# Optimization experiments

Hardware: AMD Instinct MI355X
Metric: run time of the kernel (lower is better)

## Reference

```python
import jax, jax.numpy as jnp
import numpy as np

LMAX = 2
L = LMAX + 1          # number of l channels
M = (LMAX + 1) ** 2   # 9 spherical components
C = 64                # channels per l
N = 1024              # nodes
E = 300               # num_elements (hard-coded in module)
P3, P2, P1 = 16, 4, 2 # CG path counts for correlation 3/2/1


def so3_linear(x, w, b=None):
    # x: [N, M, Cin]; w: [L, Cout, Cin]. Per-l channel mixing (equivariant),
    # bias only on the l=0 (scalar) block.
    outs = []
    for l in range(L):
        seg = x[:, l * l:(l + 1) * (l + 1), :]
        y = jnp.einsum('nmc,dc->nmd', seg, w[l])
        if l == 0 and b is not None:
            y = y + b
        outs.append(y)
    return jnp.concatenate(outs, axis=1)


def setup_inputs() -> dict:
    key = jax.random.key(0)
    ks = jax.random.split(key, 13)
    s = lambda k, shape, sc=1.0: jax.random.normal(k, shape, dtype=jnp.float32) * sc
    return {
        'irreps_x': s(ks[0], (N, M, C)),
        'atomic_numbers': jax.random.randint(ks[1], (N,), 0, 119),
        'w_fc1': s(ks[2], (L, C, C), 1.0 / np.sqrt(C)),
        'b_fc1': jnp.zeros((C,), jnp.float32),
        'U3': s(ks[3], (M, M, M, M, P3), 0.05),   # generalized CG coeffs, corr 3
        'W3': s(ks[4], (E, P3, C), 1.0 / np.sqrt(P3 * C)),
        'U2': s(ks[5], (M, M, M, P2), 0.05),      # corr 2
        'W2': s(ks[6], (E, P2, C), 1.0 / np.sqrt(P2 * C)),
        'U1': s(ks[7], (M, M, P1), 0.05),         # corr 1
        'W1': s(ks[8], (E, P1, C), 1.0 / np.sqrt(P1 * C)),
        'w_lin': s(ks[9], (L, C, C), 1.0 / np.sqrt(C)),   # e3nn Linear in dtp block
        'w_fc2': s(ks[10], (L, C, C), 1.0 / np.sqrt(C)),  # final SO3_Linear
        'b_fc2': jnp.zeros((C,), jnp.float32),
    }


def reference(irreps_x, atomic_numbers, w_fc1, b_fc1, U3, W3, U2, W2, U1, W1,
              w_lin, w_fc2, b_fc2):
    # 1) irreps_small_fc
    x = so3_linear(irreps_x, w_fc1, b_fc1)           # [N, M, C]
    # 2) permute(0, 2, 1): MACE layout [N, C, M]
    xT = jnp.transpose(x, (0, 2, 1))
    # one_hot(atomic_numbers) @ W  ==  gather of per-element weights
    a = atomic_numbers.astype(jnp.int32)
    w3 = W3[a]                                        # [N, P3, C]
    w2 = W2[a]                                        # [N, P2, C]
    w1 = W1[a]                                        # [N, P1, C]
    # MACE symmetric contraction, correlation = 3:
    # out[n,c,o,a,b] = sum_{i,p} U3[o,a,b,i,p] * w3[n,p,c] * x[n,c,i]
    z = jnp.einsum('nci,npc->ncip', xT, w3)           # [N, C, M, P3]
    out = jnp.einsum('oabip,ncip->ncoab', U3, z)      # [N, C, M, M, M]
    # fold in correlation-2 term, contract one input index
    c2 = jnp.einsum('oaip,npc->ncoai', U2, w2)        # [N, C, M, M, M]
    out = jnp.einsum('ncoai,nci->ncoa', c2 + out, xT) # [N, C, M, M]
    # fold in correlation-1 term, contract last input index
    c1 = jnp.einsum('oip,npc->ncoi', U1, w1)          # [N, C, M, M]
    out = jnp.einsum('ncoi,nci->nco', c1 + out, xT)   # [N, C, M]
    # e3nn per-irrep Linear inside EquivariantProductBasisBlock (no bias)
    out = jnp.transpose(out, (0, 2, 1))               # back2orderTmul -> [N, M, C]
    out = so3_linear(out, w_lin)
    # 3) final SO3_Linear back to input channel count
    out = so3_linear(out, w_fc2, b_fc2)
    return out                                        # [N, M, C]
```

## Files before the change

kernel.cpp:

```cpp
#include <hip/hip_runtime.h>


typedef __attribute__((ext_vector_type(8)))  _Float16 f16x8;
typedef __attribute__((ext_vector_type(16))) float    f32x16;
typedef __attribute__((ext_vector_type(4)))  float    f32x4;
typedef __attribute__((ext_vector_type(8)))  short    short8;

static __device__ __forceinline__ unsigned short f2bf(float f) {
    union { float f; unsigned u; } v; v.f = f;
    unsigned r = v.u + 0x7fffu + ((v.u >> 16) & 1u);
    return (unsigned short)(r >> 16);
}

__global__ void prep_u3w(const float* __restrict__ U3, const float* __restrict__ U2,
                         _Float16* __restrict__ U3w)
{
    int idx = blockIdx.x * 256 + threadIdx.x;
    int ks = idx / 192, r = idx % 192;
    int nt = r >> 6, l = r & 63;
    int oa = nt * 32 + (l & 31), half = l >> 5;
    f16x8 v;
    if (ks < 81) {
        int b = ks / 9, ksub = ks % 9, ip0 = ksub * 16 + half * 8;
        #pragma unroll
        for (int j = 0; j < 8; ++j) {
            float f = (oa < 81) ? U3[(oa * 9 + b) * 144 + ip0 + j] : 0.f;
            v[j] = (_Float16)f;
        }
    } else {
        int ip0 = (ks - 81) * 16 + half * 8;
        #pragma unroll
        for (int j = 0; j < 8; ++j) {
            int ip2 = ip0 + j;
            float f = (oa < 81 && ip2 < 36) ? U2[oa * 36 + ip2] : 0.f;
            v[j] = (_Float16)f;
        }
    }
    ((f16x8*)U3w)[idx] = v;
}

__global__ __launch_bounds__(768, 3) void mace_main(
    const float* __restrict__ irreps_x,
    const int*   __restrict__ atomic_numbers,
    const float* __restrict__ w_fc1,
    const float* __restrict__ b_fc1,
    const float* __restrict__ W3,
    const float* __restrict__ W2,
    const float* __restrict__ U1,
    const float* __restrict__ W1,
    const float* __restrict__ w_lin,
    const float* __restrict__ w_fc2,
    const float* __restrict__ b_fc2,
    const _Float16* __restrict__ U3w,
    float* __restrict__ out)
{
    __shared__ float xvL[2304];
    __shared__ __align__(16) unsigned char o2B[104448];
    float* const o2L = (float*)o2B;
    float* const o1L          = (float*)o2B;
    unsigned short* const XfA = (unsigned short*)(o2B + 9216);
    unsigned short* const WfA = (unsigned short*)(o2B + 28416);
    float* const yL           = (float*)(o2B + 54016);

    const int t  = threadIdx.x;
    const int n0 = blockIdx.x * 4;
    const int w  = t >> 6;
    const int l  = t & 63;
    const int kg = l >> 4;
    const int half = l >> 5;

    auto fill_Xf = [&](auto srcf) {
        for (int i = t; i < 48 * 192; i += 768) {
            int rr = i / 192, k = i % 192;
            int lh = k >> 6, c = k & 63;
            float v = 0.f;
            if (rr < 36) {
                int at = rr / 9, m = rr % 9;
                int lm = (m >= 4) ? 2 : (m >= 1 ? 1 : 0);
                if (lh == lm) v = srcf(at, m, c);
            }
            XfA[rr * 200 + k] = f2bf(v);
        }
    };
    auto fill_Wf = [&](const float* wmat) {
        for (int i = t; i < 64 * 192; i += 768) {
            int d = i / 192, k = i % 192;
            int lh = k >> 6, c = k & 63;
            WfA[d * 200 + k] = f2bf(wmat[lh * 4096 + d * 64 + c]);
        }
    };
    auto run_linear = [&](const float* bias, float* dst, bool to_global) {
        {
            int rt = w >> 2, ct = w & 3;
            int row = rt * 16 + (l & 15);
            int col = ct * 16 + (l & 15);
            short8 A[6];
            const unsigned short* ab = XfA + row * 200 + kg * 8;
            #pragma unroll
            for (int kt = 0; kt < 6; ++kt) A[kt] = *(const short8*)(ab + kt * 32);
            const unsigned short* bb = WfA + col * 200 + kg * 8;
            f32x4 acc0 = {0,0,0,0}, acc1 = {0,0,0,0};
            #pragma unroll
            for (int kt = 0; kt < 6; kt += 2) {
                short8 B0 = *(const short8*)(bb + kt * 32);
                short8 B1 = *(const short8*)(bb + (kt + 1) * 32);
                acc0 = __builtin_amdgcn_mfma_f32_16x16x32_bf16(A[kt],     B0, acc0, 0, 0, 0);
                acc1 = __builtin_amdgcn_mfma_f32_16x16x32_bf16(A[kt + 1], B1, acc1, 0, 0, 0);
            }
            f32x4 acc = acc0 + acc1;
            #pragma unroll
            for (int r = 0; r < 4; ++r) {
                int rr = rt * 16 + kg * 4 + r;
                if (rr < 36) {
                    int at = rr / 9, m = rr % 9;
                    float v = acc[r];
                    if (bias && m == 0) v += bias[col];
                    if (to_global) dst[(n0 + at) * 576 + m * 64 + col] = v;
                    else           dst[at * 576 + m * 64 + col] = v;
                }
            }
        }
    };

    fill_Xf([&](int at, int m, int c) { return irreps_x[(n0 + at) * 576 + m * 64 + c]; });
    fill_Wf(w_fc1);
    __syncthreads();
    run_linear(b_fc1, xvL, false);
    __syncthreads();

    {
        const int at = w / 3, ng = w % 3;
        const int an = atomic_numbers[n0 + at];
        const float* xa  = xvL + at * 576;
        const float* W3r = W3 + an * 1024;
        const float* W2r = W2 + an * 256;

        f16x8 s3f[2][9], s2f[2][3];
        #pragma unroll
        for (int mt = 0; mt < 2; ++mt) {
            const int c = mt * 32 + (l & 31);
            f16x8 w3h;
            #pragma unroll
            for (int j = 0; j < 8; ++j)
                w3h[j] = (_Float16)W3r[(half * 8 + j) * 64 + c];
            #pragma unroll
            for (int i = 0; i < 9; ++i) {
                _Float16 xi = (_Float16)xa[i * 64 + c];
                f16x8 xi8 = {xi, xi, xi, xi, xi, xi, xi, xi};
                s3f[mt][i] = w3h * xi8;
            }
            float w2v[4];
            #pragma unroll
            for (int p = 0; p < 4; ++p) w2v[p] = W2r[p * 64 + c];
            #pragma unroll
            for (int ks2 = 0; ks2 < 3; ++ks2) {
                f16x8 v;
                #pragma unroll
                for (int j = 0; j < 8; ++j) {
                    int ip2 = ks2 * 16 + half * 8 + j;
                    int i = ip2 >> 2;
                    float f = (i < 9) ? xa[i * 64 + c] * w2v[ip2 & 3] : 0.f;
                    v[j] = (_Float16)f;
                }
                s2f[mt][ks2] = v;
            }
        }

        f32x16 acc0 = {0.f}, acc1 = {0.f};
        const f16x8* Bp = (const f16x8*)U3w + ng * 64 + l;
        for (int b = 0; b < 9; ++b) {
            _Float16 h0 = (_Float16)xa[b * 64 + (l & 31)];
            _Float16 h1 = (_Float16)xa[b * 64 + 32 + (l & 31)];
            f16x8 xb0 = {h0, h0, h0, h0, h0, h0, h0, h0};
            f16x8 xb1 = {h1, h1, h1, h1, h1, h1, h1, h1};
            const f16x8* Bb = Bp + b * 9 * 192;
            #pragma unroll
            for (int ksub = 0; ksub < 9; ++ksub) {
                f16x8 B = Bb[ksub * 192];
                acc0 = __builtin_amdgcn_mfma_f32_32x32x16_f16(s3f[0][ksub] * xb0, B, acc0, 0, 0, 0);
                acc1 = __builtin_amdgcn_mfma_f32_32x32x16_f16(s3f[1][ksub] * xb1, B, acc1, 0, 0, 0);
            }
        }
        #pragma unroll
        for (int ks2 = 0; ks2 < 3; ++ks2) {
            f16x8 B = Bp[(81 + ks2) * 192];
            acc0 = __builtin_amdgcn_mfma_f32_32x32x16_f16(s2f[0][ks2], B, acc0, 0, 0, 0);
            acc1 = __builtin_amdgcn_mfma_f32_32x32x16_f16(s2f[1][ks2], B, acc1, 0, 0, 0);
        }

        const int oa = ng * 32 + (l & 31);
        float* o2row = o2L + (at * 96 + oa) * 68;
        #pragma unroll
        for (int q = 0; q < 4; ++q) {
            int c0 = q * 8 + half * 4;
            f32x4 v0 = {acc0[q*4+0], acc0[q*4+1], acc0[q*4+2], acc0[q*4+3]};
            f32x4 v1 = {acc1[q*4+0], acc1[q*4+1], acc1[q*4+2], acc1[q*4+3]};
            *(f32x4*)(o2row + c0)      = v0;
            *(f32x4*)(o2row + 32 + c0) = v1;
        }
    }
    __syncthreads();

    float o1v[3];
    #pragma unroll
    for (int it = 0; it < 3; ++it) {
        int i = t + it * 768;
        int at2 = i / 576, r2 = i % 576, o = r2 >> 6, c = r2 & 63;
        int an2 = atomic_numbers[n0 + at2];
        float w1a = W1[an2 * 128 + c], w1b = W1[an2 * 128 + 64 + c];
        const float* o2p = o2L + (at2 * 96 + o * 9) * 68 + c;
        float acc = 0.f, sa = 0.f, sb = 0.f;
        #pragma unroll
        for (int a = 0; a < 9; ++a)
            acc += o2p[a * 68] * xvL[at2 * 576 + a * 64 + c];
        #pragma unroll
        for (int i2 = 0; i2 < 9; ++i2) {
            float xc = xvL[at2 * 576 + i2 * 64 + c];
            sa += U1[o * 18 + i2 * 2]     * xc;
            sb += U1[o * 18 + i2 * 2 + 1] * xc;
        }
        o1v[it] = acc + sa * w1a + sb * w1b;
    }
    __syncthreads();
    #pragma unroll
    for (int it = 0; it < 3; ++it) {
        int i = t + it * 768;
        int at2 = i / 576, r2 = i % 576;
        o1L[at2 * 576 + r2] = o1v[it];
    }
    __syncthreads();

    fill_Xf([&](int at, int m, int c) { return o1L[at * 576 + m * 64 + c]; });
    fill_Wf(w_lin);
    __syncthreads();
    run_linear(nullptr, yL, false);
    __syncthreads();

    fill_Xf([&](int at, int m, int c) { return yL[at * 576 + m * 64 + c]; });
    fill_Wf(w_fc2);
    __syncthreads();
    run_linear(b_fc2, out, true);
}

extern "C" void kernel_launch(void* const* d_in, const int* in_sizes, int n_in,
                              void* d_out, int out_size, void* d_ws, size_t ws_size,
                              hipStream_t stream) {
    const float* irreps_x = (const float*)d_in[0];
    const int*   anum     = (const int*)d_in[1];
    const float* w_fc1    = (const float*)d_in[2];
    const float* b_fc1    = (const float*)d_in[3];
    const float* U3       = (const float*)d_in[4];
    const float* W3       = (const float*)d_in[5];
    const float* U2       = (const float*)d_in[6];
    const float* W2       = (const float*)d_in[7];
    const float* U1       = (const float*)d_in[8];
    const float* W1       = (const float*)d_in[9];
    const float* w_lin    = (const float*)d_in[10];
    const float* w_fc2    = (const float*)d_in[11];
    const float* b_fc2    = (const float*)d_in[12];
    float* out = (float*)d_out;

    _Float16* U3w = (_Float16*)d_ws;

    prep_u3w<<<63, 256, 0, stream>>>(U3, U2, U3w);
    mace_main<<<256, 768, 0, stream>>>(irreps_x, anum, w_fc1, b_fc1, W3, W2,
                                       U1, W1, w_lin, w_fc2, b_fc2, U3w, out);
}
```

Measured before the change: 122.4 us.

## Fuse U3 prep into main kernel, halve nodes per block, store o2 in fp16

Drops the separate prep kernel that repacked U3/U2 into fp16 MFMA layout. The main kernel now reads fp32 U3 directly and converts it in registers with cvt_pkrtz, and builds the U2 operand inline. Blocks now handle 2 nodes with 384 threads instead of 4 with 768, and the o2 intermediate is stored as fp16 in LDS, which shrinks shared memory so more blocks fit per CU. This saves a launch and raises occupancy, but each block re-reads and re-converts U3 from global memory and loses some intermediate precision.

After: 190.8 us. 55.9% more time.

```diff
diff --git a/kernel.cpp b/kernel.cpp
--- a/kernel.cpp
+++ b/kernel.cpp
@@ -2,6 +2,8 @@
 
 
 typedef __attribute__((ext_vector_type(8)))  _Float16 f16x8;
+typedef __attribute__((ext_vector_type(4)))  _Float16 f16x4;
+typedef __attribute__((ext_vector_type(2)))  __fp16   hf16x2;
 typedef __attribute__((ext_vector_type(16))) float    f32x16;
 typedef __attribute__((ext_vector_type(4)))  float    f32x4;
 typedef __attribute__((ext_vector_type(8)))  short    short8;
@@ -12,106 +14,83 @@
     return (unsigned short)(r >> 16);
 }
 
-__global__ void prep_u3w(const float* __restrict__ U3, const float* __restrict__ U2,
-                         _Float16* __restrict__ U3w)
-{
-    int idx = blockIdx.x * 256 + threadIdx.x;
-    int ks = idx / 192, r = idx % 192;
-    int nt = r >> 6, l = r & 63;
-    int oa = nt * 32 + (l & 31), half = l >> 5;
-    f16x8 v;
-    if (ks < 81) {
-        int b = ks / 9, ksub = ks % 9, ip0 = ksub * 16 + half * 8;
-        #pragma unroll
-        for (int j = 0; j < 8; ++j) {
-            float f = (oa < 81) ? U3[(oa * 9 + b) * 144 + ip0 + j] : 0.f;
-            v[j] = (_Float16)f;
-        }
-    } else {
-        int ip0 = (ks - 81) * 16 + half * 8;
-        #pragma unroll
-        for (int j = 0; j < 8; ++j) {
-            int ip2 = ip0 + j;
-            float f = (oa < 81 && ip2 < 36) ? U2[oa * 36 + ip2] : 0.f;
-            v[j] = (_Float16)f;
-        }
-    }
-    ((f16x8*)U3w)[idx] = v;
-}
-
-__global__ __launch_bounds__(768, 3) void mace_main(
+__global__ __launch_bounds__(384, 4) void mace_all(
     const float* __restrict__ irreps_x,
     const int*   __restrict__ atomic_numbers,
     const float* __restrict__ w_fc1,
     const float* __restrict__ b_fc1,
+    const float* __restrict__ U3,
     const float* __restrict__ W3,
+    const float* __restrict__ U2,
     const float* __restrict__ W2,
     const float* __restrict__ U1,
     const float* __restrict__ W1,
     const float* __restrict__ w_lin,
     const float* __restrict__ w_fc2,
     const float* __restrict__ b_fc2,
-    const _Float16* __restrict__ U3w,
     float* __restrict__ out)
 {
-    __shared__ float xvL[2304];
-    __shared__ __align__(16) unsigned char o2B[104448];
-    float* const o2L = (float*)o2B;
-    float* const o1L          = (float*)o2B;
-    unsigned short* const XfA = (unsigned short*)(o2B + 9216);
-    unsigned short* const WfA = (unsigned short*)(o2B + 28416);
-    float* const yL           = (float*)(o2B + 54016);
+    __shared__ float xvL[1152];
+    __shared__ __align__(16) unsigned char region[47616];
+    _Float16* const o2L       = (_Float16*)region;
+    float* const o1L          = (float*)region;
+    unsigned short* const XfA = (unsigned short*)(region + 4608);
+    unsigned short* const WfA = (unsigned short*)(region + 17408);
+    float* const yL           = (float*)(region + 43008);
 
     const int t  = threadIdx.x;
-    const int n0 = blockIdx.x * 4;
+    const int n0 = blockIdx.x * 2;
     const int w  = t >> 6;
     const int l  = t & 63;
     const int kg = l >> 4;
-    const int half = l >> 5;
+    const int hf = l >> 5;
+    const int c32 = l & 31;
 
     auto fill_Xf = [&](auto srcf) {
-        for (int i = t; i < 48 * 192; i += 768) {
-            int rr = i / 192, k = i % 192;
+        for (int i = t; i < 32 * 96; i += 384) {
+            int rr = i / 96, k = (i % 96) * 2;
             int lh = k >> 6, c = k & 63;
-            float v = 0.f;
-            if (rr < 36) {
+            float v0 = 0.f, v1 = 0.f;
+            if (rr < 18) {
                 int at = rr / 9, m = rr % 9;
                 int lm = (m >= 4) ? 2 : (m >= 1 ? 1 : 0);
-                if (lh == lm) v = srcf(at, m, c);
-            }
-            XfA[rr * 200 + k] = f2bf(v);
+                if (lh == lm) { v0 = srcf(at, m, c); v1 = srcf(at, m, c + 1); }
+            }
+            unsigned pk = (unsigned)f2bf(v0) | ((unsigned)f2bf(v1) << 16);
+            *(unsigned*)(XfA + rr * 200 + k) = pk;
         }
     };
     auto fill_Wf = [&](const float* wmat) {
-        for (int i = t; i < 64 * 192; i += 768) {
-            int d = i / 192, k = i % 192;
+        for (int i = t; i < 64 * 96; i += 384) {
+            int d = i / 96, k = (i % 96) * 2;
             int lh = k >> 6, c = k & 63;
-            WfA[d * 200 + k] = f2bf(wmat[lh * 4096 + d * 64 + c]);
+            const float* wp = wmat + lh * 4096 + d * 64 + c;
+            unsigned pk = (unsigned)f2bf(wp[0]) | ((unsigned)f2bf(wp[1]) << 16);
+            *(unsigned*)(WfA + d * 200 + k) = pk;
         }
     };
     auto run_linear = [&](const float* bias, float* dst, bool to_global) {
-        {
-            int rt = w >> 2, ct = w & 3;
+        for (int tile = w; tile < 8; tile += 6) {
+            int rt = tile >> 2, ct = tile & 3;
             int row = rt * 16 + (l & 15);
             int col = ct * 16 + (l & 15);
-            short8 A[6];
             const unsigned short* ab = XfA + row * 200 + kg * 8;
-            #pragma unroll
-            for (int kt = 0; kt < 6; ++kt) A[kt] = *(const short8*)(ab + kt * 32);
             const unsigned short* bb = WfA + col * 200 + kg * 8;
             f32x4 acc0 = {0,0,0,0}, acc1 = {0,0,0,0};
             #pragma unroll
             for (int kt = 0; kt < 6; kt += 2) {
+                short8 A0 = *(const short8*)(ab + kt * 32);
+                short8 A1 = *(const short8*)(ab + (kt + 1) * 32);
                 short8 B0 = *(const short8*)(bb + kt * 32);
                 short8 B1 = *(const short8*)(bb + (kt + 1) * 32);
-                acc0 = __builtin_amdgcn_mfma_f32_16x16x32_bf16(A[kt],     B0, acc0, 0, 0, 0);
-                acc1 = __builtin_amdgcn_mfma_f32_16x16x32_bf16(A[kt + 1], B1, acc1, 0, 0, 0);
+                acc0 = __builtin_amdgcn_mfma_f32_16x16x32_bf16(A0, B0, acc0, 0, 0, 0);
+                acc1 = __builtin_amdgcn_mfma_f32_16x16x32_bf16(A1, B1, acc1, 0, 0, 0);
             }
             f32x4 acc = acc0 + acc1;
             #pragma unroll
             for (int r = 0; r < 4; ++r) {
                 int rr = rt * 16 + kg * 4 + r;
-                if (rr < 36) {
+                if (rr < 18) {
                     int at = rr / 9, m = rr % 9;
                     float v = acc[r];
                     if (bias && m == 0) v += bias[col];
@@ -135,68 +114,76 @@
         const float* W3r = W3 + an * 1024;
         const float* W2r = W2 + an * 256;
 
-        f16x8 s3f[2][9], s2f[2][3];
+        f16x8 s3f[2][9];
         #pragma unroll
         for (int mt = 0; mt < 2; ++mt) {
-            const int c = mt * 32 + (l & 31);
+            const int c = mt * 32 + c32;
             f16x8 w3h;
             #pragma unroll
             for (int j = 0; j < 8; ++j)
-                w3h[j] = (_Float16)W3r[(half * 8 + j) * 64 + c];
+                w3h[j] = (_Float16)W3r[(hf * 8 + j) * 64 + c];
             #pragma unroll
             for (int i = 0; i < 9; ++i) {
                 _Float16 xi = (_Float16)xa[i * 64 + c];
                 f16x8 xi8 = {xi, xi, xi, xi, xi, xi, xi, xi};
                 s3f[mt][i] = w3h * xi8;
             }
-            float w2v[4];
-            #pragma unroll
-            for (int p = 0; p < 4; ++p) w2v[p] = W2r[p * 64 + c];
-            #pragma unroll
-            for (int ks2 = 0; ks2 < 3; ++ks2) {
-                f16x8 v;
-                #pragma unroll
-                for (int j = 0; j < 8; ++j) {
-                    int ip2 = ks2 * 16 + half * 8 + j;
-                    int i = ip2 >> 2;
-                    float f = (i < 9) ? xa[i * 64 + c] * w2v[ip2 & 3] : 0.f;
-                    v[j] = (_Float16)f;
-                }
-                s2f[mt][ks2] = v;
-            }
-        }
+        }
+
+        const int oa  = ng * 32 + c32;
+        const int oaL = (oa > 80) ? 80 : oa;
+        const float* Bb = U3 + oaL * 1296 + hf * 8;
 
         f32x16 acc0 = {0.f}, acc1 = {0.f};
-        const f16x8* Bp = (const f16x8*)U3w + ng * 64 + l;
         for (int b = 0; b < 9; ++b) {
-            _Float16 h0 = (_Float16)xa[b * 64 + (l & 31)];
-            _Float16 h1 = (_Float16)xa[b * 64 + 32 + (l & 31)];
+            _Float16 h0 = (_Float16)xa[b * 64 + c32];
+            _Float16 h1 = (_Float16)xa[b * 64 + 32 + c32];
             f16x8 xb0 = {h0, h0, h0, h0, h0, h0, h0, h0};
             f16x8 xb1 = {h1, h1, h1, h1, h1, h1, h1, h1};
-            const f16x8* Bb = Bp + b * 9 * 192;
+            const float* Bp = Bb + b * 144;
             #pragma unroll
             for (int ksub = 0; ksub < 9; ++ksub) {
-                f16x8 B = Bb[ksub * 192];
-                acc0 = __builtin_amdgcn_mfma_f32_32x32x16_f16(s3f[0][ksub] * xb0, B, acc0, 0, 0, 0);
-                acc1 = __builtin_amdgcn_mfma_f32_32x32x16_f16(s3f[1][ksub] * xb1, B, acc1, 0, 0, 0);
-            }
-        }
+                float4 f0 = *(const float4*)(Bp + ksub * 16);
+                float4 f1 = *(const float4*)(Bp + ksub * 16 + 4);
+                union { hf16x2 h2[4]; f16x8 v; } u;
+                u.h2[0] = __builtin_amdgcn_cvt_pkrtz(f0.x, f0.y);
+                u.h2[1] = __builtin_amdgcn_cvt_pkrtz(f0.z, f0.w);
+                u.h2[2] = __builtin_amdgcn_cvt_pkrtz(f1.x, f1.y);
+                u.h2[3] = __builtin_amdgcn_cvt_pkrtz(f1.z, f1.w);
+                acc0 = __builtin_amdgcn_mfma_f32_32x32x16_f16(s3f[0][ksub] * xb0, u.v, acc0, 0, 0, 0);
+                acc1 = __builtin_amdgcn_mfma_f32_32x32x16_f16(s3f[1][ksub] * xb1, u.v, acc1, 0, 0, 0);
+            }
+        }
+        const float* U2r = U2 + oaL * 36;
         #pragma unroll
         for (int ks2 = 0; ks2 < 3; ++ks2) {
-            f16x8 B = Bp[(81 + ks2) * 192];
-            acc0 = __builtin_amdgcn_mfma_f32_32x32x16_f16(s2f[0][ks2], B, acc0, 0, 0, 0);
-            acc1 = __builtin_amdgcn_mfma_f32_32x32x16_f16(s2f[1][ks2], B, acc1, 0, 0, 0);
-        }
-
-        const int oa = ng * 32 + (l & 31);
-        float* o2row = o2L + (at * 96 + oa) * 68;
+            f16x8 a0, a1, B;
+            #pragma unroll
+            for (int j = 0; j < 8; ++j) {
+                int ip2 = ks2 * 16 + hf * 8 + j;
+                int ii = ip2 >> 2, pp = ip2 & 3;
+                float f0 = 0.f, f1 = 0.f, bv = 0.f;
+                if (ii < 9) {
+                    f0 = xa[ii * 64 + c32]      * W2r[pp * 64 + c32];
+                    f1 = xa[ii * 64 + 32 + c32] * W2r[pp * 64 + 32 + c32];
+                    bv = U2r[ip2];
+                }
+                a0[j] = (_Float16)f0; a1[j] = (_Float16)f1; B[j] = (_Float16)bv;
+            }
+            acc0 = __builtin_amdgcn_mfma_f32_32x32x16_f16(a0, B, acc0, 0, 0, 0);
+            acc1 = __builtin_amdgcn_mfma_f32_32x32x16_f16(a1, B, acc1, 0, 0, 0);
+        }
+
+        _Float16* o2row = o2L + (at * 96 + oa) * 68;
         #pragma unroll
         for (int q = 0; q < 4; ++q) {
-            int c0 = q * 8 + half * 4;
-            f32x4 v0 = {acc0[q*4+0], acc0[q*4+1], acc0[q*4+2], acc0[q*4+3]};
-            f32x4 v1 = {acc1[q*4+0], acc1[q*4+1], acc1[q*4+2], acc1[q*4+3]};
-            *(f32x4*)(o2row + c0)      = v0;
-            *(f32x4*)(o2row + 32 + c0) = v1;
+            int c0 = q * 8 + hf * 4;
+            f16x4 v0 = {(_Float16)acc0[q*4+0], (_Float16)acc0[q*4+1],
+                        (_Float16)acc0[q*4+2], (_Float16)acc0[q*4+3]};
+            f16x4 v1 = {(_Float16)acc1[q*4+0], (_Float16)acc1[q*4+1],
+                        (_Float16)acc1[q*4+2], (_Float16)acc1[q*4+3]};
+            *(f16x4*)(o2row + c0)      = v0;
+            *(f16x4*)(o2row + 32 + c0) = v1;
         }
     }
     __syncthreads();
@@ -204,15 +191,15 @@
     float o1v[3];
     #pragma unroll
     for (int it = 0; it < 3; ++it) {
-        int i = t + it * 768;
+        int i = t + it * 384;
         int at2 = i / 576, r2 = i % 576, o = r2 >> 6, c = r2 & 63;
         int an2 = atomic_numbers[n0 + at2];
         float w1a = W1[an2 * 128 + c], w1b = W1[an2 * 128 + 64 + c];
-        const float* o2p = o2L + (at2 * 96 + o * 9) * 68 + c;
+        const _Float16* o2p = o2L + (at2 * 96 + o * 9) * 68 + c;
         float acc = 0.f, sa = 0.f, sb = 0.f;
         #pragma unroll
         for (int a = 0; a < 9; ++a)
-            acc += o2p[a * 68] * xvL[at2 * 576 + a * 64 + c];
+            acc += (float)o2p[a * 68] * xvL[at2 * 576 + a * 64 + c];
         #pragma unroll
         for (int i2 = 0; i2 < 9; ++i2) {
             float xc = xvL[at2 * 576 + i2 * 64 + c];
@@ -223,11 +210,7 @@
     }
     __syncthreads();
     #pragma unroll
-    for (int it = 0; it < 3; ++it) {
-        int i = t + it * 768;
-        int at2 = i / 576, r2 = i % 576;
-        o1L[at2 * 576 + r2] = o1v[it];
-    }
+    for (int it = 0; it < 3; ++it) o1L[t + it * 384] = o1v[it];
     __syncthreads();
 
     fill_Xf([&](int at, int m, int c) { return o1L[at * 576 + m * 64 + c]; });
@@ -260,9 +243,6 @@
     const float* b_fc2    = (const float*)d_in[12];
     float* out = (float*)d_out;
 
-    _Float16* U3w = (_Float16*)d_ws;
-
-    prep_u3w<<<63, 256, 0, stream>>>(U3, U2, U3w);
-    mace_main<<<256, 768, 0, stream>>>(irreps_x, anum, w_fc1, b_fc1, W3, W2,
-                                       U1, W1, w_lin, w_fc2, b_fc2, U3w, out);
+    mace_all<<<512, 384, 0, stream>>>(irreps_x, anum, w_fc1, b_fc1, U3, W3,
+                                      U2, W2, U1, W1, w_lin, w_fc2, b_fc2, out);
 }
```
